# Kernel tuning notes

Measured on AMD Instinct MI355X. Metric: run time of the kernel, lower is better.

The kernel has to match this reference:

```python
import jax, jax.numpy as jnp
import numpy as np

D_MODEL = 1024
NUM_HEADS = 16
D_K = D_MODEL // NUM_HEADS
B, T = 4, 2048


def setup_inputs() -> dict:
    key = jax.random.key(0)
    ks = jax.random.split(key, 12)
    s = 0.02
    inp = {
        "query": jax.random.normal(ks[0], (B, T, D_MODEL), jnp.float32),
        "key": jax.random.normal(ks[1], (B, T, D_MODEL), jnp.float32),
        "value": jax.random.normal(ks[2], (B, T, D_MODEL), jnp.float32),
        "mask": jnp.tril(jnp.ones((T, T), jnp.int32))[None, None],  # [1,1,T,T] causal
        "Wq": jax.random.normal(ks[3], (D_MODEL, D_MODEL), jnp.float32) * s,
        "bq": jnp.zeros((D_MODEL,), jnp.float32),
        "Wk": jax.random.normal(ks[4], (D_MODEL, D_MODEL), jnp.float32) * s,
        "bk": jnp.zeros((D_MODEL,), jnp.float32),
        "Wv": jax.random.normal(ks[5], (D_MODEL, D_MODEL), jnp.float32) * s,
        "bv": jnp.zeros((D_MODEL,), jnp.float32),
        "Wo": jax.random.normal(ks[6], (D_MODEL, D_MODEL), jnp.float32) * s,
        "bo": jnp.zeros((D_MODEL,), jnp.float32),
    }
    return inp


def reference(query, key, value, mask, Wq, bq, Wk, bk, Wv, bv, Wo, bo):
    def split_heads(x):
        # [B,T,D] -> [B,H,T,Dk]
        return x.reshape(B, T, NUM_HEADS, D_K).transpose(0, 2, 1, 3)

    q = split_heads(query @ Wq.T + bq)
    k = split_heads(key @ Wk.T + bk)
    v = split_heads(value @ Wv.T + bv)

    scale = jnp.sqrt(jnp.asarray(D_K, q.dtype))
    scores = jnp.einsum("bhqd,bhkd->bhqk", q, k) / scale  # [B,H,T,T]
    scores = jnp.where(mask == 0, jnp.asarray(-1e9, scores.dtype), scores)
    attn = jax.nn.softmax(scores, axis=-1)
    out = jnp.einsum("bhqk,bhkd->bhqd", attn, v)
    out = out.transpose(0, 2, 1, 3).reshape(B, T, D_MODEL)
    return out @ Wo.T + bo
```

## Files before the change

kernel.cpp:

```cpp
#include <hip/hip_runtime.h>
#include <hip/hip_bf16.h>

#define D_MODEL 1024
#define NHEADS  16
#define DK      64
#define BATCH   4
#define SEQ     2048
#define M_TOT   (BATCH * SEQ)

typedef __attribute__((ext_vector_type(8)))  __bf16 bf16x8;
typedef __attribute__((ext_vector_type(4)))  float  f32x4;
typedef __attribute__((ext_vector_type(16))) float  f32x16;
typedef unsigned short ushort_t;

static __device__ __forceinline__ unsigned int f2bf(float f) {
    union { float f; unsigned int i; } v; v.f = f;
    unsigned int x = v.i;
    return (x + 0x7fffu + ((x >> 16) & 1u)) >> 16;
}

static __device__ __forceinline__ void gl16(const void* g, void* lds_generic) {
    __attribute__((address_space(1))) void* gp =
        (__attribute__((address_space(1))) void*)(unsigned long long)g;
    __attribute__((address_space(3))) void* lp =
        (__attribute__((address_space(3))) void*)(unsigned int)(unsigned long long)lds_generic;
    __builtin_amdgcn_global_load_lds(gp, lp, 16, 0, 0);
}

__global__ __launch_bounds__(256) void cvt_in3(
    const float* __restrict__ i0, const float* __restrict__ i1,
    const float* __restrict__ i2,
    ushort_t* __restrict__ o0, ushort_t* __restrict__ o1,
    ushort_t* __restrict__ o2, int n8)
{
    const float* in; ushort_t* out;
    switch (blockIdx.y) {
        case 0: in = i0; out = o0; break;
        case 1: in = i1; out = o1; break;
        default: in = i2; out = o2; break;
    }
    int i = blockIdx.x * blockDim.x + threadIdx.x;
    if (i >= n8) return;
    const float4* p = (const float4*)in + (size_t)i * 2;
    float4 a = p[0], b = p[1];
    uint4 o;
    o.x = f2bf(a.x) | (f2bf(a.y) << 16);
    o.y = f2bf(a.z) | (f2bf(a.w) << 16);
    o.z = f2bf(b.x) | (f2bf(b.y) << 16);
    o.w = f2bf(b.z) | (f2bf(b.w) << 16);
    *((uint4*)out + i) = o;
}

__global__ __launch_bounds__(256) void cvt_w4(
    const float* __restrict__ w0, const float* __restrict__ w1,
    const float* __restrict__ w2, const float* __restrict__ w3,
    ushort_t* __restrict__ o0, ushort_t* __restrict__ o1,
    ushort_t* __restrict__ o2, ushort_t* __restrict__ o3, int n8)
{
    const float* w; ushort_t* o;
    switch (blockIdx.y) {
        case 0: w = w0; o = o0; break;
        case 1: w = w1; o = o1; break;
        case 2: w = w2; o = o2; break;
        default: w = w3; o = o3; break;
    }
    int i = blockIdx.x * blockDim.x + threadIdx.x;
    if (i >= n8) return;
    const float4* p = (const float4*)w + (size_t)i * 2;
    float4 a = p[0], b = p[1];
    uint4 u;
    u.x = f2bf(a.x) | (f2bf(a.y) << 16);
    u.y = f2bf(a.z) | (f2bf(a.w) << 16);
    u.z = f2bf(b.x) | (f2bf(b.y) << 16);
    u.w = f2bf(b.z) | (f2bf(b.w) << 16);
    *((uint4*)o + i) = u;
}

__global__ __launch_bounds__(256) void gemm_nt_bias(
    const ushort_t* __restrict__ A0, const ushort_t* __restrict__ A1,
    const ushort_t* __restrict__ A2,
    const ushort_t* __restrict__ B0, const ushort_t* __restrict__ B1,
    const ushort_t* __restrict__ B2,
    const float* __restrict__ b0, const float* __restrict__ b1,
    const float* __restrict__ b2,
    void* __restrict__ O0, void* __restrict__ O1, void* __restrict__ O2,
    int mode)
{
    const int z = blockIdx.z;
    const ushort_t* A  = (z == 0) ? A0 : (z == 1) ? A1 : A2;
    const ushort_t* Bt = (z == 0) ? B0 : (z == 1) ? B1 : B2;
    const float* bias  = (z == 0) ? b0 : (z == 1) ? b1 : b2;
    void* OutV         = (z == 0) ? O0 : (z == 1) ? O1 : O2;

    __shared__ ushort_t sA[128 * 64];
    __shared__ ushort_t sB[128 * 64];
    const int K    = 1024;
    const int tid  = threadIdx.x;
    const int lane = tid & 63;
    const int wave = tid >> 6;
    const int m0   = blockIdx.y * 128;
    const int n0   = blockIdx.x * 128;
    const int wrow = (wave >> 1) * 64;
    const int wcol = (wave & 1) * 64;
    const int l15  = lane & 15;
    const int quad = lane >> 4;
    const int swz  = l15 & 7;

    size_t aoffs[4], boffs[4];
#pragma unroll
    for (int i = 0; i < 4; i++) {
        int c = tid + 256 * i;
        int row = c >> 3;
        int ch  = (c & 7) ^ (row & 7);
        aoffs[i] = (size_t)(m0 + row) * K + ch * 8;
        boffs[i] = (size_t)(n0 + row) * K + ch * 8;
    }

    f32x4 acc[4][4];
#pragma unroll
    for (int i = 0; i < 4; i++)
#pragma unroll
        for (int j = 0; j < 4; j++)
#pragma unroll
            for (int r = 0; r < 4; r++) acc[i][j][r] = 0.0f;

    for (int kt = 0; kt < K; kt += 64) {
        __syncthreads();
#pragma unroll
        for (int i = 0; i < 4; i++) {
            int c = tid + 256 * i;
            gl16(A + aoffs[i] + kt, &sA[c * 8]);
            gl16(Bt + boffs[i] + kt, &sB[c * 8]);
        }
        __syncthreads();

#pragma unroll
        for (int kk = 0; kk < 2; kk++) {
            bf16x8 afr[4], bfr[4];
            const int chp = ((kk * 4 + quad) ^ swz) * 8;
#pragma unroll
            for (int i = 0; i < 4; i++)
                afr[i] = *(const bf16x8*)(&sA[(wrow + i * 16 + l15) * 64 + chp]);
#pragma unroll
            for (int j = 0; j < 4; j++)
                bfr[j] = *(const bf16x8*)(&sB[(wcol + j * 16 + l15) * 64 + chp]);
#pragma unroll
            for (int i = 0; i < 4; i++)
#pragma unroll
                for (int j = 0; j < 4; j++)
                    acc[i][j] = __builtin_amdgcn_mfma_f32_16x16x32_bf16(
                        afr[i], bfr[j], acc[i][j], 0, 0, 0);
        }
    }

#pragma unroll
    for (int j = 0; j < 4; j++) {
        int col  = n0 + wcol + j * 16 + l15;
        float bv = bias[col];
#pragma unroll
        for (int i = 0; i < 4; i++) {
#pragma unroll
            for (int r = 0; r < 4; r++) {
                int row = m0 + wrow + i * 16 + quad * 4 + r;
                float o = acc[i][j][r] + bv;
                if (mode == 0) {
                    ((ushort_t*)OutV)[(size_t)row * 1024 + col] = (ushort_t)f2bf(o);
                } else if (mode == 1) {
                    int b = row >> 11, t = row & 2047;
                    int h = col >> 6,  dk = col & 63;
                    ((ushort_t*)OutV)[((size_t)(b * 16 + h) * 2048 + t) * 64 + dk] =
                        (ushort_t)f2bf(o);
                } else {
                    ((float*)OutV)[(size_t)row * 1024 + col] = o;
                }
            }
        }
    }
}

__global__ __launch_bounds__(256) void transpose_v(
    const ushort_t* __restrict__ in, ushort_t* __restrict__ out)
{
    __shared__ ushort_t sT[64 * 65];
    const int tid = threadIdx.x;
    const int bh  = blockIdx.y;
    const int t0  = blockIdx.x * 64;
    const size_t ibase = ((size_t)bh * SEQ + t0) * 64;
    const size_t obase = (size_t)bh * 64 * SEQ + t0;

#pragma unroll
    for (int i = 0; i < 2; i++) {
        int c  = tid + 256 * i;
        int t  = c >> 3;
        int d0 = (c & 7) * 8;
        int4 v = *(const int4*)(&in[ibase + (size_t)t * 64 + d0]);
        const ushort_t* e = (const ushort_t*)&v;
#pragma unroll
        for (int j = 0; j < 8; j++) sT[(d0 + j) * 65 + t] = e[j];
    }
    __syncthreads();
#pragma unroll
    for (int i = 0; i < 2; i++) {
        int c  = tid + 256 * i;
        int d  = c >> 3;
        int tb = (c & 7) * 8;
        ushort_t tmp[8];
#pragma unroll
        for (int j = 0; j < 8; j++) tmp[j] = sT[d * 65 + tb + j];
        *(int4*)(&out[obase + (size_t)d * SEQ + tb]) = *(const int4*)tmp;
    }
}

__global__ __launch_bounds__(256, 2) void attn_causal(
    const ushort_t* __restrict__ Q,
    const ushort_t* __restrict__ Km,
    const ushort_t* __restrict__ Vt,
    ushort_t* __restrict__ O)
{
    __shared__ ushort_t sK[2][128 * 64];
    __shared__ ushort_t sVt[2][64 * 128];

    const int tid  = threadIdx.x;
    const int lane = tid & 63;
    const int wave = tid >> 6;
    const int l31  = lane & 31;
    const int hi   = lane >> 5;
    const int bh   = blockIdx.x;
    const int pi   = blockIdx.y;
    const int usplit = 15 - pi;
    const size_t base = (size_t)bh * SEQ * 64;

    size_t ksrc[4], vsrc[4];
#pragma unroll
    for (int i = 0; i < 4; i++) {
        int c  = tid + 256 * i;
        int kr = c >> 3, kc = (c & 7) ^ (kr & 7);
        ksrc[i] = base + (size_t)kr * 64 + kc * 8;
        int vr = c >> 4, vc = (c & 15) ^ (vr & 7);
        vsrc[i] = base + (size_t)vr * SEQ + vc * 8;
    }

    bf16x8 qfr[4];
    f32x16 oacc[2];
    float  lsum;

    auto zacc = [&]() {
#pragma unroll
        for (int j = 0; j < 2; j++)
#pragma unroll
            for (int r = 0; r < 16; r++) oacc[j][r] = 0.0f;
        lsum = 0.0f;
    };

    auto loadQ = [&](int qtile) {
        const size_t qrow = base + (size_t)(qtile * 128 + wave * 32 + l31) * 64;
#pragma unroll
        for (int kk = 0; kk < 4; kk++)
            qfr[kk] = *(const bf16x8*)&Q[qrow + kk * 16 + hi * 8];
    };

    auto stage = [&](int buf, int s) {
        const size_t ko = (size_t)s * 128 * 64;
        const size_t vo = (size_t)s * 128;
#pragma unroll
        for (int i = 0; i < 4; i++) {
            int c = tid + 256 * i;
            gl16(Km + ksrc[i] + ko, &sK[buf][c * 8]);
            gl16(Vt + vsrc[i] + vo, &sVt[buf][c * 8]);
        }
    };

    const float SC2 = 0.18033688f;
    const float C2  = 17.3123405f;

    auto compute = [&](int cur, int kvt, bool diag, int qtile) {
        const ushort_t* kb_ = &sK[cur][0];
        const ushort_t* vb_ = &sVt[cur][0];
        const int qg  = qtile * 128 + wave * 32 + l31;
        const int kv0 = kvt * 128;
#pragma unroll
        for (int b = 0; b < 4; b++) {
            f32x16 sacc;
#pragma unroll
            for (int r = 0; r < 16; r++) sacc[r] = 0.0f;
            const int krow = b * 32 + l31;
            const int ksw  = krow & 7;
            __builtin_amdgcn_s_setprio(1);
#pragma unroll
            for (int kk = 0; kk < 4; kk++) {
                bf16x8 afr = *(const bf16x8*)&kb_[krow * 64 + (((kk * 2 + hi) ^ ksw) * 8)];
                sacc = __builtin_amdgcn_mfma_f32_32x32x16_bf16(afr, qfr[kk], sacc, 0, 0, 0);
            }
            __builtin_amdgcn_s_setprio(0);

            float p[16];
#pragma unroll
            for (int r = 0; r < 16; r++) {
                float v = fmaf(sacc[r], SC2, -C2);
                if (diag) {
                    int kvg = kv0 + b * 32 + (r & 3) + 8 * (r >> 2) + 4 * hi;
                    if (kvg > qg) v = -INFINITY;
                }
                float e = __builtin_amdgcn_exp2f(v);
                p[r] = e;
                lsum += e;
            }

            unsigned w[8];
#pragma unroll
            for (int t = 0; t < 4; t++) {
                asm("v_cvt_pk_bf16_f32 %0, %1, %2"
                    : "=v"(w[2 * t]) : "v"(p[4 * t]), "v"(p[4 * t + 1]));
                asm("v_cvt_pk_bf16_f32 %0, %1, %2"
                    : "=v"(w[2 * t + 1]) : "v"(p[4 * t + 2]), "v"(p[4 * t + 3]));
            }

#pragma unroll
            for (int kb = 0; kb < 2; kb++) {
                unsigned aA = w[kb * 4 + 0], bA = w[kb * 4 + 2];
                unsigned aB = w[kb * 4 + 1], bB = w[kb * 4 + 3];
                asm("v_permlane32_swap_b32 %0, %1" : "+v"(aA), "+v"(bA));
                asm("v_permlane32_swap_b32 %0, %1" : "+v"(aB), "+v"(bB));
                union { unsigned u[4]; bf16x8 v8; } fr;
                fr.u[0] = aA; fr.u[1] = aB; fr.u[2] = bA; fr.u[3] = bB;
                __builtin_amdgcn_s_setprio(1);
#pragma unroll
                for (int j = 0; j < 2; j++) {
                    const int vrow = j * 32 + l31;
                    bf16x8 bfr = *(const bf16x8*)&vb_[
                        vrow * 128 + (((b * 4 + kb * 2 + hi) ^ (vrow & 7)) * 8)];
                    oacc[j] = __builtin_amdgcn_mfma_f32_32x32x16_bf16(
                        fr.v8, bfr, oacc[j], 0, 0, 0);
                }
                __builtin_amdgcn_s_setprio(0);
            }
        }
    };

    const int ob = bh >> 4, oh = bh & 15;
    auto epilogue = [&](int qtile) {
        float tot = lsum + __shfl_xor(lsum, 32);
        float inv = 1.0f / tot;
#pragma unroll
        for (int r = 0; r < 16; r++) {
            int qloc = (r & 3) + 8 * (r >> 2) + 4 * hi;
            float invr = __shfl(inv, qloc);
            int qg2 = qtile * 128 + wave * 32 + qloc;
#pragma unroll
            for (int j = 0; j < 2; j++) {
                O[((size_t)(ob * SEQ) + qg2) * 1024 + oh * 64 + j * 32 + l31] =
                    (ushort_t)f2bf(oacc[j][r] * invr);
            }
        }
    };

    zacc();
    loadQ(usplit);
    int qtile = usplit;
    stage(0, 0);
    asm volatile("s_waitcnt vmcnt(0)");
    __syncthreads();
    int cur = 0;
    for (int u = 0; u <= 16; ++u) {
        if (u < 16) {
            int un = u + 1;
            int sn = (un <= usplit) ? un : (un - usplit - 1);
            stage(cur ^ 1, sn);
        }
        int sc = (u <= usplit) ? u : (u - usplit - 1);
        bool diag = (u == usplit) || (u == 16);
        compute(cur, sc, diag, qtile);
        if (u == usplit) {
            epilogue(qtile);
            zacc();
            qtile = pi;
            loadQ(pi);
        }
        asm volatile("s_waitcnt vmcnt(0)");
        __syncthreads();
        cur ^= 1;
    }
    epilogue(qtile);
}

extern "C" void kernel_launch(void* const* d_in, const int* in_sizes, int n_in,
                              void* d_out, int out_size, void* d_ws, size_t ws_size,
                              hipStream_t stream) {
    const float* q_in = (const float*)d_in[0];
    const float* k_in = (const float*)d_in[1];
    const float* v_in = (const float*)d_in[2];
    const float* Wq = (const float*)d_in[4];
    const float* bq = (const float*)d_in[5];
    const float* Wk = (const float*)d_in[6];
    const float* bk = (const float*)d_in[7];
    const float* Wv = (const float*)d_in[8];
    const float* bv = (const float*)d_in[9];
    const float* Wo = (const float*)d_in[10];
    const float* bo = (const float*)d_in[11];

    ushort_t* ws = (ushort_t*)d_ws;
    const size_t TEN = (size_t)M_TOT * D_MODEL;
    const size_t WEL = (size_t)D_MODEL * D_MODEL;
    ushort_t* tmp = ws;
    ushort_t* WqB = ws + TEN;
    ushort_t* WkB = WqB + WEL;
    ushort_t* WvB = WkB + WEL;
    ushort_t* WoB = WvB + WEL;
    ushort_t* qw  = WoB + WEL;
    ushort_t* kw  = qw + TEN;
    ushort_t* vw  = kw + TEN;
    ushort_t* ow  = vw + TEN;
    ushort_t* vstage = (ushort_t*)d_out;

    dim3 bb(256);
    const int n8_in = (int)(TEN / 8);
    const int n8_w  = (int)(WEL / 8);

    cvt_w4<<<dim3(n8_w / 256, 4), bb, 0, stream>>>(Wq, Wk, Wv, Wo, WqB, WkB, WvB, WoB, n8_w);
    cvt_in3<<<dim3(n8_in / 256, 3), bb, 0, stream>>>(q_in, k_in, v_in, tmp, ow, vstage, n8_in);

    gemm_nt_bias<<<dim3(D_MODEL / 128, M_TOT / 128, 3), bb, 0, stream>>>(
        tmp, ow, vstage, WqB, WkB, WvB, bq, bk, bv, qw, kw, vw, 1);

    transpose_v<<<dim3(SEQ / 64, BATCH * NHEADS), bb, 0, stream>>>(vw, tmp);

    attn_causal<<<dim3(BATCH * NHEADS, 8), bb, 0, stream>>>(qw, kw, tmp, ow);

    gemm_nt_bias<<<dim3(D_MODEL / 128, M_TOT / 128, 1), bb, 0, stream>>>(
        ow, ow, ow, WoB, WoB, WoB, bo, bo, bo, d_out, d_out, d_out, 2);
}
```

Measured before the change: 362.2 us.

## Double-buffer GEMM LDS, remap tiles, and fuse V transpose into projection epilogue

The projection GEMM now prefetches the next K-tile into a second LDS buffer while computing the current one, and it remaps block indices so tiles sharing operands run close together. The V projection writes its output directly in transposed [b,h,dk,t] layout, which removes the separate transpose kernel and its extra global round trip. The extra LDS buffer doubles shared memory per block and may reduce occupancy.

New measurement: 319.0 us. 1.14x faster.

```diff
diff --git a/kernel.cpp b/kernel.cpp
--- a/kernel.cpp
+++ b/kernel.cpp
@@ -92,14 +92,18 @@
     const float* bias  = (z == 0) ? b0 : (z == 1) ? b1 : b2;
     void* OutV         = (z == 0) ? O0 : (z == 1) ? O1 : O2;
 
-    __shared__ ushort_t sA[128 * 64];
-    __shared__ ushort_t sB[128 * 64];
+    __shared__ ushort_t sA[2][128 * 64];
+    __shared__ ushort_t sB[2][128 * 64];
     const int K    = 1024;
     const int tid  = threadIdx.x;
     const int lane = tid & 63;
     const int wave = tid >> 6;
-    const int m0   = blockIdx.y * 128;
-    const int n0   = blockIdx.x * 128;
+
+    const int flat = (int)blockIdx.x + 8 * (int)blockIdx.y;
+    const int nf   = (flat & 7) * 64 + (flat >> 3);
+    const int m0   = (nf >> 3) * 128;
+    const int n0   = (nf & 7) * 128;
+
     const int wrow = (wave >> 1) * 64;
     const int wcol = (wave & 1) * 64;
     const int l15  = lane & 15;
@@ -124,15 +128,22 @@
 #pragma unroll
             for (int r = 0; r < 4; r++) acc[i][j][r] = 0.0f;
 
-    for (int kt = 0; kt < K; kt += 64) {
-        __syncthreads();
+    auto stage = [&](int buf, int kt) {
 #pragma unroll
         for (int i = 0; i < 4; i++) {
             int c = tid + 256 * i;
-            gl16(A + aoffs[i] + kt, &sA[c * 8]);
-            gl16(Bt + boffs[i] + kt, &sB[c * 8]);
-        }
-        __syncthreads();
+            gl16(A + aoffs[i] + kt, &sA[buf][c * 8]);
+            gl16(Bt + boffs[i] + kt, &sB[buf][c * 8]);
+        }
+    };
+
+    stage(0, 0);
+    asm volatile("s_waitcnt vmcnt(0)");
+    __syncthreads();
+    int cur = 0;
+
+    for (int kt = 0; kt < K; kt += 64) {
+        if (kt + 64 < K) stage(cur ^ 1, kt + 64);
 
 #pragma unroll
         for (int kk = 0; kk < 2; kk++) {
@@ -140,10 +151,10 @@
             const int chp = ((kk * 4 + quad) ^ swz) * 8;
 #pragma unroll
             for (int i = 0; i < 4; i++)
-                afr[i] = *(const bf16x8*)(&sA[(wrow + i * 16 + l15) * 64 + chp]);
+                afr[i] = *(const bf16x8*)(&sA[cur][(wrow + i * 16 + l15) * 64 + chp]);
 #pragma unroll
             for (int j = 0; j < 4; j++)
-                bfr[j] = *(const bf16x8*)(&sB[(wcol + j * 16 + l15) * 64 + chp]);
+                bfr[j] = *(const bf16x8*)(&sB[cur][(wcol + j * 16 + l15) * 64 + chp]);
 #pragma unroll
             for (int i = 0; i < 4; i++)
 #pragma unroll
@@ -151,6 +162,31 @@
                     acc[i][j] = __builtin_amdgcn_mfma_f32_16x16x32_bf16(
                         afr[i], bfr[j], acc[i][j], 0, 0, 0);
         }
+
+        asm volatile("s_waitcnt vmcnt(0)");
+        __syncthreads();
+        cur ^= 1;
+    }
+
+    if (mode == 1 && z == 2) {
+#pragma unroll
+        for (int j = 0; j < 4; j++) {
+            int col  = n0 + wcol + j * 16 + l15;
+            float bv = bias[col];
+            int h = col >> 6, dk = col & 63;
+#pragma unroll
+            for (int i = 0; i < 4; i++) {
+                int row0 = m0 + wrow + i * 16 + quad * 4;
+                int b = row0 >> 11, t0 = row0 & 2047;
+                ushort_t pk[4];
+#pragma unroll
+                for (int r = 0; r < 4; r++)
+                    pk[r] = (ushort_t)f2bf(acc[i][j][r] + bv);
+                *(uint2*)&((ushort_t*)OutV)[((size_t)(b * 16 + h) * 64 + dk) * SEQ + t0] =
+                    *(const uint2*)pk;
+            }
+        }
+        return;
     }
 
 #pragma unroll
@@ -175,39 +211,6 @@
                 }
             }
         }
-    }
-}
-
-__global__ __launch_bounds__(256) void transpose_v(
-    const ushort_t* __restrict__ in, ushort_t* __restrict__ out)
-{
-    __shared__ ushort_t sT[64 * 65];
-    const int tid = threadIdx.x;
-    const int bh  = blockIdx.y;
-    const int t0  = blockIdx.x * 64;
-    const size_t ibase = ((size_t)bh * SEQ + t0) * 64;
-    const size_t obase = (size_t)bh * 64 * SEQ + t0;
-
-#pragma unroll
-    for (int i = 0; i < 2; i++) {
-        int c  = tid + 256 * i;
-        int t  = c >> 3;
-        int d0 = (c & 7) * 8;
-        int4 v = *(const int4*)(&in[ibase + (size_t)t * 64 + d0]);
-        const ushort_t* e = (const ushort_t*)&v;
-#pragma unroll
-        for (int j = 0; j < 8; j++) sT[(d0 + j) * 65 + t] = e[j];
-    }
-    __syncthreads();
-#pragma unroll
-    for (int i = 0; i < 2; i++) {
-        int c  = tid + 256 * i;
-        int d  = c >> 3;
-        int tb = (c & 7) * 8;
-        ushort_t tmp[8];
-#pragma unroll
-        for (int j = 0; j < 8; j++) tmp[j] = sT[d * 65 + tb + j];
-        *(int4*)(&out[obase + (size_t)d * SEQ + tb]) = *(const int4*)tmp;
     }
 }
 
@@ -422,9 +425,7 @@
     gemm_nt_bias<<<dim3(D_MODEL / 128, M_TOT / 128, 3), bb, 0, stream>>>(
         tmp, ow, vstage, WqB, WkB, WvB, bq, bk, bv, qw, kw, vw, 1);
 
-    transpose_v<<<dim3(SEQ / 64, BATCH * NHEADS), bb, 0, stream>>>(vw, tmp);
-
-    attn_causal<<<dim3(BATCH * NHEADS, 8), bb, 0, stream>>>(qw, kw, tmp, ow);
+    attn_causal<<<dim3(BATCH * NHEADS, 8), bb, 0, stream>>>(qw, kw, vw, ow);
 
     gemm_nt_bias<<<dim3(D_MODEL / 128, M_TOT / 128, 1), bb, 0, stream>>>(
         ow, ow, ow, WoB, WoB, WoB, bo, bo, bo, d_out, d_out, d_out, 2);
```
